# Optimization experiments

Measured on AMD Instinct MI355X. Metric: run time of the kernel, lower is better.

## Reference

```python
import jax, jax.numpy as jnp
import numpy as np

S, A, B, D = 4, 64, 2048, 384
H1, H2, H3 = 128, 128, 64


def setup_inputs() -> dict:
    key = jax.random.key(0)
    ks = jax.random.split(key, 6)
    x = jax.random.normal(ks[0], (B, A, D), dtype=jnp.float32)
    species = jax.random.randint(ks[1], (A,), 0, S, dtype=jnp.int32)
    # per-species stacked MLP weights, scaled ~1/sqrt(fan_in) like reset_parameters
    W0 = jax.random.normal(ks[2], (S, D, H1), dtype=jnp.float32) / np.sqrt(D)
    W1 = jax.random.normal(ks[3], (S, H1, H2), dtype=jnp.float32) / np.sqrt(H1)
    W2 = jax.random.normal(ks[4], (S, H2, H3), dtype=jnp.float32) / np.sqrt(H2)
    W3 = jax.random.normal(ks[5], (S, H3, 1), dtype=jnp.float32) / np.sqrt(H3)
    b0 = jnp.zeros((S, H1), jnp.float32)
    b1 = jnp.zeros((S, H2), jnp.float32)
    b2 = jnp.zeros((S, H3), jnp.float32)
    b3 = jnp.zeros((S, 1), jnp.float32)
    return {"x": x, "species": species, "W0": W0, "b0": b0, "W1": W1,
            "b1": b1, "W2": W2, "b2": b2, "W3": W3, "b3": b3}


def reference(x, species, W0, b0, W1, b1, W2, b2, W3, b3):
    # Gather per-atom species weights once, then batched per-atom GEMMs.
    # x: [B, A, D]; species: [A]
    y = jnp.einsum('bad,adh->bah', x, W0[species]) + b0[species]
    y = jnp.exp(-y * y)
    y = jnp.einsum('bah,ahk->bak', y, W1[species]) + b1[species]
    y = jnp.exp(-y * y)
    y = jnp.einsum('bak,akm->bam', y, W2[species]) + b2[species]
    y = jnp.exp(-y * y)
    y = jnp.einsum('bam,amo->bao', y, W3[species]) + b3[species]  # [B, A, 1]
    return jnp.squeeze(jnp.sum(y, axis=1))  # [B]
```

## Files before the change

### kernel.cpp

```cpp
#include <hip/hip_runtime.h>

#define S_DIM 4
#define A_DIM 64
#define B_DIM 2048
#define D_DIM 384
#define H1D 128
#define H2D 128
#define H3D 64
#define MT 64
#define XROW (A_DIM * D_DIM)

typedef __attribute__((ext_vector_type(8))) short short8;
typedef __attribute__((ext_vector_type(4))) float float4v;

__device__ __forceinline__ unsigned short f2bf(float f) {
  unsigned u = __float_as_uint(f);
  u += 0x7FFFu + ((u >> 16) & 1u);
  return (unsigned short)(u >> 16);
}

__device__ __forceinline__ void store_bf4(unsigned short* p, float4v v) {
  union { unsigned short s[4]; uint2 u; } t;
  t.s[0] = f2bf(v[0]); t.s[1] = f2bf(v[1]);
  t.s[2] = f2bf(v[2]); t.s[3] = f2bf(v[3]);
  *(uint2*)p = t.u;
}

#define LGKM_BARRIER()                                        \
  do {                                                        \
    asm volatile("s_waitcnt lgkmcnt(0)" ::: "memory");        \
    __builtin_amdgcn_s_barrier();                             \
    asm volatile("" ::: "memory");                            \
  } while (0)

__global__ __launch_bounds__(256) void prep_weights(
    const float* __restrict__ W0, const float* __restrict__ W1,
    const float* __restrict__ W2,
    unsigned short* __restrict__ W0T, unsigned short* __restrict__ W1T,
    unsigned short* __restrict__ W2T) {
  __shared__ float tile[32][33];
  int b = blockIdx.x;
  const float* src; unsigned short* dst; int R, C, dt, ht, s;
  if (b < 192) {
    s = b / 48; int t = b % 48; dt = t / 4; ht = t % 4;
    src = W0 + s * D_DIM * H1D; dst = W0T + s * H1D * D_DIM; R = D_DIM; C = H1D;
  } else if (b < 256) {
    int bb = b - 192; s = bb / 16; int t = bb % 16; dt = t / 4; ht = t % 4;
    src = W1 + s * H1D * H2D; dst = W1T + s * H2D * H1D; R = H1D; C = H2D;
  } else {
    int bb = b - 256; s = bb / 8; int t = bb % 8; dt = t / 2; ht = t % 2;
    src = W2 + s * H2D * H3D; dst = W2T + s * H3D * H2D; R = H2D; C = H3D;
  }
  int tx = threadIdx.x & 31, ty = threadIdx.x >> 5;
#pragma unroll
  for (int k = 0; k < 4; ++k)
    tile[ty + 8 * k][tx] = src[(size_t)(dt * 32 + ty + 8 * k) * C + ht * 32 + tx];
  __syncthreads();
#pragma unroll
  for (int k = 0; k < 4; ++k)
    dst[(size_t)(ht * 32 + ty + 8 * k) * R + dt * 32 + tx] = f2bf(tile[tx][ty + 8 * k]);
}

__global__ __launch_bounds__(256, 3) void mlp_fused(
    const float* __restrict__ x, const int* __restrict__ species,
    const unsigned short* __restrict__ W0T, const unsigned short* __restrict__ W1T,
    const unsigned short* __restrict__ W2T,
    const float* __restrict__ b0, const float* __restrict__ b1,
    const float* __restrict__ b2, const float* __restrict__ W3,
    const float* __restrict__ b3, float* __restrict__ partial) {
  __shared__ __align__(16) unsigned short xbuf0[MT * 136];
  __shared__ __align__(16) unsigned short xbuf1[MT * 136];
  __shared__ float W3s[H3D];
  unsigned short* H0 = xbuf1;
  unsigned short* H1 = xbuf0;
  float* H2 = (float*)xbuf1;

  const int a = blockIdx.x;
  const int brow0 = blockIdx.y * MT;
  const int sp = species[a];
  const int tid = threadIdx.x;
  const int wave = tid >> 6;
  const int lane = tid & 63;
  const int q = lane >> 4;
  const int r = lane & 15;

  const float4v zero = {0.f, 0.f, 0.f, 0.f};

  const int srow16 = tid >> 4;
  const int c16 = tid & 15;
  const float* xbase = x + ((size_t)(brow0 + srow16) * A_DIM + a) * D_DIM + c16 * 4;
  unsigned short* xd0 = xbuf0 + srow16 * 136 + c16 * 4;
  unsigned short* xd1 = xbuf1 + srow16 * 136 + c16 * 4;
  const unsigned short* w0base =
      W0T + (size_t)sp * H1D * D_DIM + (wave * 32 + r) * D_DIM + q * 8;

  float4v xv[8], xw[8];
#pragma unroll
  for (int h = 0; h < 4; ++h) {
    xv[2 * h]     = *(const float4v*)(xbase + (size_t)h * 16 * XROW);
    xv[2 * h + 1] = *(const float4v*)(xbase + (size_t)h * 16 * XROW + 64);
  }
#pragma unroll
  for (int h = 0; h < 4; ++h) {
    xw[2 * h]     = *(const float4v*)(xbase + (size_t)h * 16 * XROW + 128);
    xw[2 * h + 1] = *(const float4v*)(xbase + (size_t)h * 16 * XROW + 192);
  }
  if (tid < H3D) W3s[tid] = W3[sp * H3D + tid];
  short8 bf[4][2];
#pragma unroll
  for (int kk = 0; kk < 4; ++kk)
#pragma unroll
    for (int n = 0; n < 2; ++n)
      bf[kk][n] = *(const short8*)(w0base + n * 16 * D_DIM + kk * 32);
#pragma unroll
  for (int h = 0; h < 4; ++h) {
    store_bf4(xd0 + h * 16 * 136, xv[2 * h]);
    store_bf4(xd0 + h * 16 * 136 + 64, xv[2 * h + 1]);
  }
  LGKM_BARRIER();

  float4v acc0[4][2];
#pragma unroll
  for (int g = 0; g < 4; ++g) { acc0[g][0] = zero; acc0[g][1] = zero; }

#pragma unroll
  for (int h = 0; h < 4; ++h) {
    store_bf4(xd1 + h * 16 * 136, xw[2 * h]);
    store_bf4(xd1 + h * 16 * 136 + 64, xw[2 * h + 1]);
  }
#pragma unroll
  for (int h = 0; h < 4; ++h) {
    xw[2 * h]     = *(const float4v*)(xbase + (size_t)h * 16 * XROW + 256);
    xw[2 * h + 1] = *(const float4v*)(xbase + (size_t)h * 16 * XROW + 320);
  }
#pragma unroll
  for (int g = 0; g < 4; ++g)
#pragma unroll
    for (int kk = 0; kk < 4; ++kk) {
      short8 af = *(const short8*)(xbuf0 + (g * 16 + r) * 136 + kk * 32 + q * 8);
      acc0[g][0] = __builtin_amdgcn_mfma_f32_16x16x32_bf16(af, bf[kk][0], acc0[g][0], 0, 0, 0);
      acc0[g][1] = __builtin_amdgcn_mfma_f32_16x16x32_bf16(af, bf[kk][1], acc0[g][1], 0, 0, 0);
    }
  LGKM_BARRIER();

#pragma unroll
  for (int kk = 0; kk < 4; ++kk)
#pragma unroll
    for (int n = 0; n < 2; ++n)
      bf[kk][n] = *(const short8*)(w0base + n * 16 * D_DIM + 128 + kk * 32);
#pragma unroll
  for (int g = 0; g < 4; ++g)
#pragma unroll
    for (int kk = 0; kk < 4; ++kk) {
      short8 af = *(const short8*)(xbuf1 + (g * 16 + r) * 136 + kk * 32 + q * 8);
      acc0[g][0] = __builtin_amdgcn_mfma_f32_16x16x32_bf16(af, bf[kk][0], acc0[g][0], 0, 0, 0);
      acc0[g][1] = __builtin_amdgcn_mfma_f32_16x16x32_bf16(af, bf[kk][1], acc0[g][1], 0, 0, 0);
    }
#pragma unroll
  for (int h = 0; h < 4; ++h) {
    store_bf4(xd0 + h * 16 * 136, xw[2 * h]);
    store_bf4(xd0 + h * 16 * 136 + 64, xw[2 * h + 1]);
  }
  LGKM_BARRIER();

#pragma unroll
  for (int kk = 0; kk < 4; ++kk)
#pragma unroll
    for (int n = 0; n < 2; ++n)
      bf[kk][n] = *(const short8*)(w0base + n * 16 * D_DIM + 256 + kk * 32);
#pragma unroll
  for (int g = 0; g < 4; ++g)
#pragma unroll
    for (int kk = 0; kk < 4; ++kk) {
      short8 af = *(const short8*)(xbuf0 + (g * 16 + r) * 136 + kk * 32 + q * 8);
      acc0[g][0] = __builtin_amdgcn_mfma_f32_16x16x32_bf16(af, bf[kk][0], acc0[g][0], 0, 0, 0);
      acc0[g][1] = __builtin_amdgcn_mfma_f32_16x16x32_bf16(af, bf[kk][1], acc0[g][1], 0, 0, 0);
    }
  {
    const float* b0p = b0 + sp * H1D;
#pragma unroll
    for (int n = 0; n < 2; ++n) {
      float bias = b0p[wave * 32 + n * 16 + r];
#pragma unroll
      for (int g = 0; g < 4; ++g)
#pragma unroll
        for (int i = 0; i < 4; ++i) {
          float y = acc0[g][n][i] + bias;
          H0[(g * 16 + q * 4 + i) * 136 + wave * 32 + n * 16 + r] = f2bf(__expf(-y * y));
        }
    }
  }
  __syncthreads();

  {
    float4v acc1[4][2];
#pragma unroll
    for (int g = 0; g < 4; ++g) { acc1[g][0] = zero; acc1[g][1] = zero; }
    const unsigned short* w1base =
        W1T + (size_t)sp * H2D * H1D + (wave * 32 + r) * H1D + q * 8;
    short8 wf[4][2];
#pragma unroll
    for (int kk = 0; kk < 4; ++kk)
#pragma unroll
      for (int n = 0; n < 2; ++n)
        wf[kk][n] = *(const short8*)(w1base + n * 16 * H1D + kk * 32);
#pragma unroll
    for (int g = 0; g < 4; ++g)
#pragma unroll
      for (int kk = 0; kk < 4; ++kk) {
        short8 af = *(const short8*)(H0 + (g * 16 + r) * 136 + kk * 32 + q * 8);
        acc1[g][0] = __builtin_amdgcn_mfma_f32_16x16x32_bf16(af, wf[kk][0], acc1[g][0], 0, 0, 0);
        acc1[g][1] = __builtin_amdgcn_mfma_f32_16x16x32_bf16(af, wf[kk][1], acc1[g][1], 0, 0, 0);
      }
    const float* b1p = b1 + sp * H2D;
#pragma unroll
    for (int n = 0; n < 2; ++n) {
      float bias = b1p[wave * 32 + n * 16 + r];
#pragma unroll
      for (int g = 0; g < 4; ++g)
#pragma unroll
        for (int i = 0; i < 4; ++i) {
          float y = acc1[g][n][i] + bias;
          H1[(g * 16 + q * 4 + i) * 136 + wave * 32 + n * 16 + r] = f2bf(__expf(-y * y));
        }
    }
  }
  __syncthreads();

  {
    float4v acc2[4];
#pragma unroll
    for (int g = 0; g < 4; ++g) acc2[g] = zero;
    const unsigned short* w2base =
        W2T + (size_t)sp * H3D * H2D + (wave * 16 + r) * H2D + q * 8;
    short8 wf[4];
#pragma unroll
    for (int kk = 0; kk < 4; ++kk)
      wf[kk] = *(const short8*)(w2base + kk * 32);
#pragma unroll
    for (int g = 0; g < 4; ++g)
#pragma unroll
      for (int kk = 0; kk < 4; ++kk) {
        short8 af = *(const short8*)(H1 + (g * 16 + r) * 136 + kk * 32 + q * 8);
        acc2[g] = __builtin_amdgcn_mfma_f32_16x16x32_bf16(af, wf[kk], acc2[g], 0, 0, 0);
      }
    float bias = b2[sp * H3D + wave * 16 + r];
#pragma unroll
    for (int g = 0; g < 4; ++g)
#pragma unroll
      for (int i = 0; i < 4; ++i) {
        float y = acc2[g][i] + bias;
        H2[(g * 16 + q * 4 + i) * 68 + wave * 16 + r] = __expf(-y * y);
      }
  }
  __syncthreads();

  {
    const int row = tid >> 2;
    const int seg = tid & 3;
    const float4v* h2p = (const float4v*)(H2 + row * 68 + seg * 16);
    const float4v* w3p = (const float4v*)(W3s + seg * 16);
    float4v sv = zero;
#pragma unroll
    for (int jj = 0; jj < 4; ++jj) sv += h2p[jj] * w3p[jj];
    float s = sv[0] + sv[1] + sv[2] + sv[3];
    s += __shfl_xor(s, 1);
    s += __shfl_xor(s, 2);
    if (seg == 0) partial[(size_t)a * B_DIM + brow0 + row] = s + b3[sp];
  }
}

__global__ __launch_bounds__(256) void reduce_partial(
    const float* __restrict__ p, float* __restrict__ out) {
  const int b = blockIdx.x * 256 + threadIdx.x;
  float s = 0.f;
#pragma unroll
  for (int a = 0; a < A_DIM; ++a) s += p[(size_t)a * B_DIM + b];
  out[b] = s;
}

extern "C" void kernel_launch(void* const* d_in, const int* in_sizes, int n_in,
                              void* d_out, int out_size, void* d_ws, size_t ws_size,
                              hipStream_t stream) {
  const float* x       = (const float*)d_in[0];
  const int*   species = (const int*)d_in[1];
  const float* W0 = (const float*)d_in[2];
  const float* b0 = (const float*)d_in[3];
  const float* W1 = (const float*)d_in[4];
  const float* b1 = (const float*)d_in[5];
  const float* W2 = (const float*)d_in[6];
  const float* b2 = (const float*)d_in[7];
  const float* W3 = (const float*)d_in[8];
  const float* b3 = (const float*)d_in[9];
  float* out = (float*)d_out;

  unsigned short* W0T = (unsigned short*)d_ws;
  unsigned short* W1T = W0T + S_DIM * H1D * D_DIM;
  unsigned short* W2T = W1T + S_DIM * H2D * H1D;
  float* partial = (float*)(W2T + S_DIM * H3D * H2D);

  prep_weights<<<dim3(288), dim3(256), 0, stream>>>(W0, W1, W2, W0T, W1T, W2T);
  mlp_fused<<<dim3(A_DIM, B_DIM / MT), dim3(256), 0, stream>>>(
      x, species, W0T, W1T, W2T, b0, b1, b2, W3, b3, partial);
  reduce_partial<<<dim3(B_DIM / 256), dim3(256), 0, stream>>>(partial, out);
}
```

Before: 324.6 us.

## Give each wave its own 16-row tile and drop block-wide barriers

Each wave now owns 16 batch rows and computes all output columns of every layer, with x loaded straight from global memory into bf16 MFMA A-fragments instead of being staged through shared memory. Block-level __syncthreads are replaced by per-wave LDS waitcnt fences, and occupancy is raised to 4 blocks per SM. The aim is to remove barrier stalls and LDS staging of x. In exchange, every wave re-reads the full weight matrices from global/L2 (four times the weight traffic per block), and the x loads become strided per-lane 32-byte reads.

```diff
diff --git a/kernel.cpp b/kernel.cpp
--- a/kernel.cpp
+++ b/kernel.cpp
@@ -19,19 +19,16 @@
   return (unsigned short)(u >> 16);
 }
 
-__device__ __forceinline__ void store_bf4(unsigned short* p, float4v v) {
-  union { unsigned short s[4]; uint2 u; } t;
-  t.s[0] = f2bf(v[0]); t.s[1] = f2bf(v[1]);
-  t.s[2] = f2bf(v[2]); t.s[3] = f2bf(v[3]);
-  *(uint2*)p = t.u;
-}
-
-#define LGKM_BARRIER()                                        \
-  do {                                                        \
-    asm volatile("s_waitcnt lgkmcnt(0)" ::: "memory");        \
-    __builtin_amdgcn_s_barrier();                             \
-    asm volatile("" ::: "memory");                            \
-  } while (0)
+__device__ __forceinline__ short8 pack_bf8(float4v lo, float4v hi) {
+  short8 o;
+  o[0] = (short)f2bf(lo[0]); o[1] = (short)f2bf(lo[1]);
+  o[2] = (short)f2bf(lo[2]); o[3] = (short)f2bf(lo[3]);
+  o[4] = (short)f2bf(hi[0]); o[5] = (short)f2bf(hi[1]);
+  o[6] = (short)f2bf(hi[2]); o[7] = (short)f2bf(hi[3]);
+  return o;
+}
+
+#define WAVE_LDS_FENCE() asm volatile("s_waitcnt lgkmcnt(0)" ::: "memory")
 
 __global__ __launch_bounds__(256) void prep_weights(
     const float* __restrict__ W0, const float* __restrict__ W1,
@@ -61,212 +58,137 @@
     dst[(size_t)(ht * 32 + ty + 8 * k) * R + dt * 32 + tx] = f2bf(tile[tx][ty + 8 * k]);
 }
 
-__global__ __launch_bounds__(256, 3) void mlp_fused(
+__global__ __launch_bounds__(256, 4) void mlp_fused(
     const float* __restrict__ x, const int* __restrict__ species,
     const unsigned short* __restrict__ W0T, const unsigned short* __restrict__ W1T,
     const unsigned short* __restrict__ W2T,
     const float* __restrict__ b0, const float* __restrict__ b1,
     const float* __restrict__ b2, const float* __restrict__ W3,
     const float* __restrict__ b3, float* __restrict__ partial) {
-  __shared__ __align__(16) unsigned short xbuf0[MT * 136];
-  __shared__ __align__(16) unsigned short xbuf1[MT * 136];
-  __shared__ float W3s[H3D];
-  unsigned short* H0 = xbuf1;
-  unsigned short* H1 = xbuf0;
-  float* H2 = (float*)xbuf1;
+  __shared__ __align__(16) unsigned short Hb0[4 * 16 * 136];
+  __shared__ __align__(16) unsigned short Hb1[4 * 16 * 136];
 
   const int a = blockIdx.x;
   const int brow0 = blockIdx.y * MT;
   const int sp = species[a];
   const int tid = threadIdx.x;
-  const int wave = tid >> 6;
+  const int w = tid >> 6;
   const int lane = tid & 63;
   const int q = lane >> 4;
   const int r = lane & 15;
 
+  unsigned short* H0w = Hb1 + w * 16 * 136;
+  unsigned short* H1w = Hb0 + w * 16 * 136;
+  float* H2w = (float*)(Hb1 + w * 16 * 136);
+
   const float4v zero = {0.f, 0.f, 0.f, 0.f};
 
-  const int srow16 = tid >> 4;
-  const int c16 = tid & 15;
-  const float* xbase = x + ((size_t)(brow0 + srow16) * A_DIM + a) * D_DIM + c16 * 4;
-  unsigned short* xd0 = xbuf0 + srow16 * 136 + c16 * 4;
-  unsigned short* xd1 = xbuf1 + srow16 * 136 + c16 * 4;
-  const unsigned short* w0base =
-      W0T + (size_t)sp * H1D * D_DIM + (wave * 32 + r) * D_DIM + q * 8;
-
-  float4v xv[8], xw[8];
-#pragma unroll
-  for (int h = 0; h < 4; ++h) {
-    xv[2 * h]     = *(const float4v*)(xbase + (size_t)h * 16 * XROW);
-    xv[2 * h + 1] = *(const float4v*)(xbase + (size_t)h * 16 * XROW + 64);
-  }
-#pragma unroll
-  for (int h = 0; h < 4; ++h) {
-    xw[2 * h]     = *(const float4v*)(xbase + (size_t)h * 16 * XROW + 128);
-    xw[2 * h + 1] = *(const float4v*)(xbase + (size_t)h * 16 * XROW + 192);
-  }
-  if (tid < H3D) W3s[tid] = W3[sp * H3D + tid];
-  short8 bf[4][2];
-#pragma unroll
-  for (int kk = 0; kk < 4; ++kk)
-#pragma unroll
-    for (int n = 0; n < 2; ++n)
-      bf[kk][n] = *(const short8*)(w0base + n * 16 * D_DIM + kk * 32);
-#pragma unroll
-  for (int h = 0; h < 4; ++h) {
-    store_bf4(xd0 + h * 16 * 136, xv[2 * h]);
-    store_bf4(xd0 + h * 16 * 136 + 64, xv[2 * h + 1]);
-  }
-  LGKM_BARRIER();
-
-  float4v acc0[4][2];
-#pragma unroll
-  for (int g = 0; g < 4; ++g) { acc0[g][0] = zero; acc0[g][1] = zero; }
-
-#pragma unroll
-  for (int h = 0; h < 4; ++h) {
-    store_bf4(xd1 + h * 16 * 136, xw[2 * h]);
-    store_bf4(xd1 + h * 16 * 136 + 64, xw[2 * h + 1]);
-  }
-#pragma unroll
-  for (int h = 0; h < 4; ++h) {
-    xw[2 * h]     = *(const float4v*)(xbase + (size_t)h * 16 * XROW + 256);
-    xw[2 * h + 1] = *(const float4v*)(xbase + (size_t)h * 16 * XROW + 320);
-  }
-#pragma unroll
-  for (int g = 0; g < 4; ++g)
-#pragma unroll
-    for (int kk = 0; kk < 4; ++kk) {
-      short8 af = *(const short8*)(xbuf0 + (g * 16 + r) * 136 + kk * 32 + q * 8);
-      acc0[g][0] = __builtin_amdgcn_mfma_f32_16x16x32_bf16(af, bf[kk][0], acc0[g][0], 0, 0, 0);
-      acc0[g][1] = __builtin_amdgcn_mfma_f32_16x16x32_bf16(af, bf[kk][1], acc0[g][1], 0, 0, 0);
-    }
-  LGKM_BARRIER();
-
-#pragma unroll
-  for (int kk = 0; kk < 4; ++kk)
-#pragma unroll
-    for (int n = 0; n < 2; ++n)
-      bf[kk][n] = *(const short8*)(w0base + n * 16 * D_DIM + 128 + kk * 32);
-#pragma unroll
-  for (int g = 0; g < 4; ++g)
-#pragma unroll
-    for (int kk = 0; kk < 4; ++kk) {
-      short8 af = *(const short8*)(xbuf1 + (g * 16 + r) * 136 + kk * 32 + q * 8);
-      acc0[g][0] = __builtin_amdgcn_mfma_f32_16x16x32_bf16(af, bf[kk][0], acc0[g][0], 0, 0, 0);
-      acc0[g][1] = __builtin_amdgcn_mfma_f32_16x16x32_bf16(af, bf[kk][1], acc0[g][1], 0, 0, 0);
-    }
-#pragma unroll
-  for (int h = 0; h < 4; ++h) {
-    store_bf4(xd0 + h * 16 * 136, xw[2 * h]);
-    store_bf4(xd0 + h * 16 * 136 + 64, xw[2 * h + 1]);
-  }
-  LGKM_BARRIER();
-
-#pragma unroll
-  for (int kk = 0; kk < 4; ++kk)
-#pragma unroll
-    for (int n = 0; n < 2; ++n)
-      bf[kk][n] = *(const short8*)(w0base + n * 16 * D_DIM + 256 + kk * 32);
-#pragma unroll
-  for (int g = 0; g < 4; ++g)
-#pragma unroll
-    for (int kk = 0; kk < 4; ++kk) {
-      short8 af = *(const short8*)(xbuf0 + (g * 16 + r) * 136 + kk * 32 + q * 8);
-      acc0[g][0] = __builtin_amdgcn_mfma_f32_16x16x32_bf16(af, bf[kk][0], acc0[g][0], 0, 0, 0);
-      acc0[g][1] = __builtin_amdgcn_mfma_f32_16x16x32_bf16(af, bf[kk][1], acc0[g][1], 0, 0, 0);
-    }
-  {
+  {
+    const float* xb = x + ((size_t)(brow0 + w * 16 + r) * A_DIM + a) * D_DIM + q * 8;
+    const unsigned short* w0b = W0T + (size_t)sp * H1D * D_DIM + r * D_DIM + q * 8;
+    float4v acc0[8];
+#pragma unroll
+    for (int n = 0; n < 8; ++n) acc0[n] = zero;
+#pragma unroll
+    for (int c = 0; c < 3; ++c) {
+      short8 af[4];
+#pragma unroll
+      for (int kk = 0; kk < 4; ++kk) {
+        float4v lo = *(const float4v*)(xb + c * 128 + kk * 32);
+        float4v hi = *(const float4v*)(xb + c * 128 + kk * 32 + 4);
+        af[kk] = pack_bf8(lo, hi);
+      }
+#pragma unroll
+      for (int n = 0; n < 8; ++n)
+#pragma unroll
+        for (int kk = 0; kk < 4; ++kk) {
+          short8 wf = *(const short8*)(w0b + (size_t)n * 16 * D_DIM + c * 128 + kk * 32);
+          acc0[n] = __builtin_amdgcn_mfma_f32_16x16x32_bf16(af[kk], wf, acc0[n], 0, 0, 0);
+        }
+    }
     const float* b0p = b0 + sp * H1D;
 #pragma unroll
-    for (int n = 0; n < 2; ++n) {
-      float bias = b0p[wave * 32 + n * 16 + r];
-#pragma unroll
-      for (int g = 0; g < 4; ++g)
-#pragma unroll
-        for (int i = 0; i < 4; ++i) {
-          float y = acc0[g][n][i] + bias;
-          H0[(g * 16 + q * 4 + i) * 136 + wave * 32 + n * 16 + r] = f2bf(__expf(-y * y));
-        }
-    }
-  }
-  __syncthreads();
-
-  {
-    float4v acc1[4][2];
-#pragma unroll
-    for (int g = 0; g < 4; ++g) { acc1[g][0] = zero; acc1[g][1] = zero; }
-    const unsigned short* w1base =
-        W1T + (size_t)sp * H2D * H1D + (wave * 32 + r) * H1D + q * 8;
-    short8 wf[4][2];
+    for (int n = 0; n < 8; ++n) {
+      float bias = b0p[n * 16 + r];
+#pragma unroll
+      for (int i = 0; i < 4; ++i) {
+        float y = acc0[n][i] + bias;
+        H0w[(q * 4 + i) * 136 + n * 16 + r] = f2bf(__expf(-y * y));
+      }
+    }
+  }
+  WAVE_LDS_FENCE();
+
+  {
+    const unsigned short* w1b = W1T + (size_t)sp * H2D * H1D + r * H1D + q * 8;
+    float4v acc1[8];
+#pragma unroll
+    for (int n = 0; n < 8; ++n) acc1[n] = zero;
+    short8 af[4];
 #pragma unroll
     for (int kk = 0; kk < 4; ++kk)
-#pragma unroll
-      for (int n = 0; n < 2; ++n)
-        wf[kk][n] = *(const short8*)(w1base + n * 16 * H1D + kk * 32);
-#pragma unroll
-    for (int g = 0; g < 4; ++g)
+      af[kk] = *(const short8*)(H0w + r * 136 + kk * 32 + q * 8);
+#pragma unroll
+    for (int n = 0; n < 8; ++n)
 #pragma unroll
       for (int kk = 0; kk < 4; ++kk) {
-        short8 af = *(const short8*)(H0 + (g * 16 + r) * 136 + kk * 32 + q * 8);
-        acc1[g][0] = __builtin_amdgcn_mfma_f32_16x16x32_bf16(af, wf[kk][0], acc1[g][0], 0, 0, 0);
-        acc1[g][1] = __builtin_amdgcn_mfma_f32_16x16x32_bf16(af, wf[kk][1], acc1[g][1], 0, 0, 0);
+        short8 wf = *(const short8*)(w1b + (size_t)n * 16 * H1D + kk * 32);
+        acc1[n] = __builtin_amdgcn_mfma_f32_16x16x32_bf16(af[kk], wf, acc1[n], 0, 0, 0);
       }
     const float* b1p = b1 + sp * H2D;
 #pragma unroll
-    for (int n = 0; n < 2; ++n) {
-      float bias = b1p[wave * 32 + n * 16 + r];
-#pragma unroll
-      for (int g = 0; g < 4; ++g)
-#pragma unroll
-        for (int i = 0; i < 4; ++i) {
-          float y = acc1[g][n][i] + bias;
-          H1[(g * 16 + q * 4 + i) * 136 + wave * 32 + n * 16 + r] = f2bf(__expf(-y * y));
-        }
-    }
-  }
-  __syncthreads();
-
-  {
+    for (int n = 0; n < 8; ++n) {
+      float bias = b1p[n * 16 + r];
+#pragma unroll
+      for (int i = 0; i < 4; ++i) {
+        float y = acc1[n][i] + bias;
+        H1w[(q * 4 + i) * 136 + n * 16 + r] = f2bf(__expf(-y * y));
+      }
+    }
+  }
+  WAVE_LDS_FENCE();
+
+  {
+    const unsigned short* w2b = W2T + (size_t)sp * H3D * H2D + r * H2D + q * 8;
     float4v acc2[4];
 #pragma unroll
-    for (int g = 0; g < 4; ++g) acc2[g] = zero;
-    const unsigned short* w2base =
-        W2T + (size_t)sp * H3D * H2D + (wave * 16 + r) * H2D + q * 8;
-    short8 wf[4];
+    for (int n = 0; n < 4; ++n) acc2[n] = zero;
+    short8 af[4];
 #pragma unroll
     for (int kk = 0; kk < 4; ++kk)
-      wf[kk] = *(const short8*)(w2base + kk * 32);
-#pragma unroll
-    for (int g = 0; g < 4; ++g)
+      af[kk] = *(const short8*)(H1w + r * 136 + kk * 32 + q * 8);
+#pragma unroll
+    for (int n = 0; n < 4; ++n)
 #pragma unroll
       for (int kk = 0; kk < 4; ++kk) {
-        short8 af = *(const short8*)(H1 + (g * 16 + r) * 136 + kk * 32 + q * 8);
-        acc2[g] = __builtin_amdgcn_mfma_f32_16x16x32_bf16(af, wf[kk], acc2[g], 0, 0, 0);
-      }
-    float bias = b2[sp * H3D + wave * 16 + r];
-#pragma unroll
-    for (int g = 0; g < 4; ++g)
+        short8 wf = *(const short8*)(w2b + (size_t)n * 16 * H2D + kk * 32);
+        acc2[n] = __builtin_amdgcn_mfma_f32_16x16x32_bf16(af[kk], wf, acc2[n], 0, 0, 0);
+      }
+    const float* b2p = b2 + sp * H3D;
+#pragma unroll
+    for (int n = 0; n < 4; ++n) {
+      float bias = b2p[n * 16 + r];
 #pragma unroll
       for (int i = 0; i < 4; ++i) {
-        float y = acc2[g][i] + bias;
-        H2[(g * 16 + q * 4 + i) * 68 + wave * 16 + r] = __expf(-y * y);
-      }
-  }
-  __syncthreads();
-
-  {
-    const int row = tid >> 2;
-    const int seg = tid & 3;
-    const float4v* h2p = (const float4v*)(H2 + row * 68 + seg * 16);
-    const float4v* w3p = (const float4v*)(W3s + seg * 16);
+        float y = acc2[n][i] + bias;
+        H2w[(q * 4 + i) * 68 + n * 16 + r] = __expf(-y * y);
+      }
+    }
+  }
+  WAVE_LDS_FENCE();
+
+  {
+    const int row = lane >> 2;
+    const int seg = lane & 3;
+    const float4v* h2p = (const float4v*)(H2w + row * 68 + seg * 16);
+    const float4v* w3p = (const float4v*)(W3 + sp * H3D + seg * 16);
     float4v sv = zero;
 #pragma unroll
     for (int jj = 0; jj < 4; ++jj) sv += h2p[jj] * w3p[jj];
     float s = sv[0] + sv[1] + sv[2] + sv[3];
     s += __shfl_xor(s, 1);
     s += __shfl_xor(s, 2);
-    if (seg == 0) partial[(size_t)a * B_DIM + brow0 + row] = s + b3[sp];
+    if (seg == 0) partial[(size_t)a * B_DIM + brow0 + w * 16 + row] = s + b3[sp];
   }
 }
 
```

After: 394.3 us. 21.5% more time.

## Load all x chunks upfront into triple LDS buffer and prefetch weights

Applied to the files above, without the earlier changes.

Issues all three 128-column chunks of x as global loads at kernel start and stores them into three separate LDS buffers behind one barrier. The staged two-buffer ping-pong and its intermediate barriers are removed. The layer-0 GEMM then loops over the chunks with double-buffered register prefetch of W0 fragments. The aim is more memory requests in flight and fewer barriers. In exchange, LDS per block grows by about half and VGPR pressure rises under the 3-block launch bound, which risks occupancy loss or spills.

```diff
diff --git a/kernel.cpp b/kernel.cpp
--- a/kernel.cpp
+++ b/kernel.cpp
@@ -9,6 +9,7 @@
 #define H3D 64
 #define MT 64
 #define XROW (A_DIM * D_DIM)
+#define CH (MT * 136)
 
 typedef __attribute__((ext_vector_type(8))) short short8;
 typedef __attribute__((ext_vector_type(4))) float float4v;
@@ -25,13 +26,6 @@
   t.s[2] = f2bf(v[2]); t.s[3] = f2bf(v[3]);
   *(uint2*)p = t.u;
 }
-
-#define LGKM_BARRIER()                                        \
-  do {                                                        \
-    asm volatile("s_waitcnt lgkmcnt(0)" ::: "memory");        \
-    __builtin_amdgcn_s_barrier();                             \
-    asm volatile("" ::: "memory");                            \
-  } while (0)
 
 __global__ __launch_bounds__(256) void prep_weights(
     const float* __restrict__ W0, const float* __restrict__ W1,
@@ -68,12 +62,11 @@
     const float* __restrict__ b0, const float* __restrict__ b1,
     const float* __restrict__ b2, const float* __restrict__ W3,
     const float* __restrict__ b3, float* __restrict__ partial) {
-  __shared__ __align__(16) unsigned short xbuf0[MT * 136];
-  __shared__ __align__(16) unsigned short xbuf1[MT * 136];
+  __shared__ __align__(16) unsigned short xs[3 * CH];
   __shared__ float W3s[H3D];
-  unsigned short* H0 = xbuf1;
-  unsigned short* H1 = xbuf0;
-  float* H2 = (float*)xbuf1;
+  unsigned short* H0 = xs;
+  unsigned short* H1 = xs + CH;
+  float* H2 = (float*)(xs + 2 * CH);
 
   const int a = blockIdx.x;
   const int brow0 = blockIdx.y * MT;
@@ -89,93 +82,75 @@
   const int srow16 = tid >> 4;
   const int c16 = tid & 15;
   const float* xbase = x + ((size_t)(brow0 + srow16) * A_DIM + a) * D_DIM + c16 * 4;
-  unsigned short* xd0 = xbuf0 + srow16 * 136 + c16 * 4;
-  unsigned short* xd1 = xbuf1 + srow16 * 136 + c16 * 4;
+  unsigned short* xd = xs + srow16 * 136 + c16 * 4;
+
+  float4v xv[8], xw[8], xz[8];
+#pragma unroll
+  for (int h = 0; h < 4; ++h) {
+    xv[2 * h]     = *(const float4v*)(xbase + (size_t)h * 16 * XROW);
+    xv[2 * h + 1] = *(const float4v*)(xbase + (size_t)h * 16 * XROW + 64);
+  }
+#pragma unroll
+  for (int h = 0; h < 4; ++h) {
+    xw[2 * h]     = *(const float4v*)(xbase + (size_t)h * 16 * XROW + 128);
+    xw[2 * h + 1] = *(const float4v*)(xbase + (size_t)h * 16 * XROW + 192);
+  }
+#pragma unroll
+  for (int h = 0; h < 4; ++h) {
+    xz[2 * h]     = *(const float4v*)(xbase + (size_t)h * 16 * XROW + 256);
+    xz[2 * h + 1] = *(const float4v*)(xbase + (size_t)h * 16 * XROW + 320);
+  }
+  if (tid < H3D) W3s[tid] = W3[sp * H3D + tid];
+#pragma unroll
+  for (int h = 0; h < 4; ++h) {
+    store_bf4(xd + h * 16 * 136, xv[2 * h]);
+    store_bf4(xd + h * 16 * 136 + 64, xv[2 * h + 1]);
+  }
+#pragma unroll
+  for (int h = 0; h < 4; ++h) {
+    store_bf4(xd + CH + h * 16 * 136, xw[2 * h]);
+    store_bf4(xd + CH + h * 16 * 136 + 64, xw[2 * h + 1]);
+  }
+#pragma unroll
+  for (int h = 0; h < 4; ++h) {
+    store_bf4(xd + 2 * CH + h * 16 * 136, xz[2 * h]);
+    store_bf4(xd + 2 * CH + h * 16 * 136 + 64, xz[2 * h + 1]);
+  }
+  __syncthreads();
+
   const unsigned short* w0base =
       W0T + (size_t)sp * H1D * D_DIM + (wave * 32 + r) * D_DIM + q * 8;
-
-  float4v xv[8], xw[8];
-#pragma unroll
-  for (int h = 0; h < 4; ++h) {
-    xv[2 * h]     = *(const float4v*)(xbase + (size_t)h * 16 * XROW);
-    xv[2 * h + 1] = *(const float4v*)(xbase + (size_t)h * 16 * XROW + 64);
-  }
-#pragma unroll
-  for (int h = 0; h < 4; ++h) {
-    xw[2 * h]     = *(const float4v*)(xbase + (size_t)h * 16 * XROW + 128);
-    xw[2 * h + 1] = *(const float4v*)(xbase + (size_t)h * 16 * XROW + 192);
-  }
-  if (tid < H3D) W3s[tid] = W3[sp * H3D + tid];
-  short8 bf[4][2];
+  float4v acc0[4][2];
+#pragma unroll
+  for (int g = 0; g < 4; ++g) { acc0[g][0] = zero; acc0[g][1] = zero; }
+  short8 bf[2][4][2];
 #pragma unroll
   for (int kk = 0; kk < 4; ++kk)
 #pragma unroll
     for (int n = 0; n < 2; ++n)
-      bf[kk][n] = *(const short8*)(w0base + n * 16 * D_DIM + kk * 32);
-#pragma unroll
-  for (int h = 0; h < 4; ++h) {
-    store_bf4(xd0 + h * 16 * 136, xv[2 * h]);
-    store_bf4(xd0 + h * 16 * 136 + 64, xv[2 * h + 1]);
-  }
-  LGKM_BARRIER();
-
-  float4v acc0[4][2];
-#pragma unroll
-  for (int g = 0; g < 4; ++g) { acc0[g][0] = zero; acc0[g][1] = zero; }
-
-#pragma unroll
-  for (int h = 0; h < 4; ++h) {
-    store_bf4(xd1 + h * 16 * 136, xw[2 * h]);
-    store_bf4(xd1 + h * 16 * 136 + 64, xw[2 * h + 1]);
-  }
-#pragma unroll
-  for (int h = 0; h < 4; ++h) {
-    xw[2 * h]     = *(const float4v*)(xbase + (size_t)h * 16 * XROW + 256);
-    xw[2 * h + 1] = *(const float4v*)(xbase + (size_t)h * 16 * XROW + 320);
-  }
-#pragma unroll
-  for (int g = 0; g < 4; ++g)
-#pragma unroll
-    for (int kk = 0; kk < 4; ++kk) {
-      short8 af = *(const short8*)(xbuf0 + (g * 16 + r) * 136 + kk * 32 + q * 8);
-      acc0[g][0] = __builtin_amdgcn_mfma_f32_16x16x32_bf16(af, bf[kk][0], acc0[g][0], 0, 0, 0);
-      acc0[g][1] = __builtin_amdgcn_mfma_f32_16x16x32_bf16(af, bf[kk][1], acc0[g][1], 0, 0, 0);
+      bf[0][kk][n] = *(const short8*)(w0base + n * 16 * D_DIM + kk * 32);
+#pragma unroll
+  for (int c = 0; c < 3; ++c) {
+    if (c < 2) {
+#pragma unroll
+      for (int kk = 0; kk < 4; ++kk)
+#pragma unroll
+        for (int n = 0; n < 2; ++n)
+          bf[(c + 1) & 1][kk][n] =
+              *(const short8*)(w0base + n * 16 * D_DIM + (c + 1) * 128 + kk * 32);
     }
-  LGKM_BARRIER();
-
-#pragma unroll
-  for (int kk = 0; kk < 4; ++kk)
-#pragma unroll
-    for (int n = 0; n < 2; ++n)
-      bf[kk][n] = *(const short8*)(w0base + n * 16 * D_DIM + 128 + kk * 32);
-#pragma unroll
-  for (int g = 0; g < 4; ++g)
-#pragma unroll
-    for (int kk = 0; kk < 4; ++kk) {
-      short8 af = *(const short8*)(xbuf1 + (g * 16 + r) * 136 + kk * 32 + q * 8);
-      acc0[g][0] = __builtin_amdgcn_mfma_f32_16x16x32_bf16(af, bf[kk][0], acc0[g][0], 0, 0, 0);
-      acc0[g][1] = __builtin_amdgcn_mfma_f32_16x16x32_bf16(af, bf[kk][1], acc0[g][1], 0, 0, 0);
-    }
-#pragma unroll
-  for (int h = 0; h < 4; ++h) {
-    store_bf4(xd0 + h * 16 * 136, xw[2 * h]);
-    store_bf4(xd0 + h * 16 * 136 + 64, xw[2 * h + 1]);
-  }
-  LGKM_BARRIER();
-
-#pragma unroll
-  for (int kk = 0; kk < 4; ++kk)
-#pragma unroll
-    for (int n = 0; n < 2; ++n)
-      bf[kk][n] = *(const short8*)(w0base + n * 16 * D_DIM + 256 + kk * 32);
-#pragma unroll
-  for (int g = 0; g < 4; ++g)
-#pragma unroll
-    for (int kk = 0; kk < 4; ++kk) {
-      short8 af = *(const short8*)(xbuf0 + (g * 16 + r) * 136 + kk * 32 + q * 8);
-      acc0[g][0] = __builtin_amdgcn_mfma_f32_16x16x32_bf16(af, bf[kk][0], acc0[g][0], 0, 0, 0);
-      acc0[g][1] = __builtin_amdgcn_mfma_f32_16x16x32_bf16(af, bf[kk][1], acc0[g][1], 0, 0, 0);
-    }
+    const unsigned short* xc = xs + c * CH;
+#pragma unroll
+    for (int g = 0; g < 4; ++g)
+#pragma unroll
+      for (int kk = 0; kk < 4; ++kk) {
+        short8 af = *(const short8*)(xc + (g * 16 + r) * 136 + kk * 32 + q * 8);
+        acc0[g][0] = __builtin_amdgcn_mfma_f32_16x16x32_bf16(af, bf[c & 1][kk][0], acc0[g][0], 0, 0, 0);
+        acc0[g][1] = __builtin_amdgcn_mfma_f32_16x16x32_bf16(af, bf[c & 1][kk][1], acc0[g][1], 0, 0, 0);
+      }
+  }
+  __syncthreads();
+
   {
     const float* b0p = b0 + sp * H1D;
 #pragma unroll
```

Result: no change. 328.3 us (+1.1%).
